# Optimization experiments

Hardware: AMD Instinct MI355X
Metric: run time of the kernel (lower is better)

The kernel has to match this reference:

```python
import math
import jax, jax.numpy as jnp
import numpy as np

B, S, H, E, F = 4, 2048, 1024, 8, 2048
CAPACITY_FACTOR = 1.25


def setup_inputs() -> dict:
    key = jax.random.key(0)
    ks = jax.random.split(key, 5)
    x = jax.random.normal(ks[0], (B, S, H), dtype=jnp.float32)
    gate_w = jax.random.normal(ks[1], (H, E), dtype=jnp.float32) * 0.02
    w1 = jax.random.normal(ks[2], (E, H, F), dtype=jnp.float32) * 0.02
    w2 = jax.random.normal(ks[3], (E, F, H), dtype=jnp.float32) * 0.02
    w3 = jax.random.normal(ks[4], (E, H, F), dtype=jnp.float32) * 0.02
    return {"x": x, "gate_w": gate_w, "w1": w1, "w2": w2, "w3": w3}


def reference(x, gate_w, w1, w2, w3):
    b, s, h = x.shape
    T = b * s
    e = gate_w.shape[1]
    xf = x.reshape(T, h)                           # [T, H]
    logits = xf @ gate_w                           # [T, E]
    capacity = min(math.ceil(T / e * CAPACITY_FACTOR), T)
    # Expert-choice: each expert picks its top-`capacity` tokens.
    scores, idx = jax.lax.top_k(logits.T, capacity)  # both [E, C]
    # Per-expert softmax over the selected tokens (dim=0 of the column vector in torch == capacity axis here).
    weights = jax.nn.softmax(scores, axis=1)       # [E, C]
    gathered = xf[idx]                             # [E, C, H]
    # Grouped SwiGLU FFN
    a = jnp.einsum('ech,ehf->ecf', gathered, w1)
    g = jnp.einsum('ech,ehf->ecf', gathered, w3)
    hidden = jax.nn.silu(a) * g                    # [E, C, F]
    out_e = jnp.einsum('ecf,efh->ech', hidden, w2) # [E, C, H]
    out_e = out_e * weights[..., None]
    # Weighted scatter-add combine
    yf = jnp.zeros((T, h), dtype=x.dtype).at[idx.reshape(-1)].add(
        out_e.reshape(-1, h))
    return yf.reshape(b, s, h), jnp.float32(0.0)
```

## Files before the change

### kernel.cpp

```cpp
#include <hip/hip_runtime.h>
#include <stdint.h>

typedef unsigned short ushort_t;
typedef __bf16 bf16x8 __attribute__((ext_vector_type(8)));
typedef float f32x4 __attribute__((ext_vector_type(4)));

#define T_TOK 8192
#define HDIM  1024
#define EXP   8
#define FDIM  2048
#define CAP   1280

__device__ __forceinline__ unsigned short f2b(float f) {
  unsigned u = __float_as_uint(f);
  u = (u + 0x7fffu + ((u >> 16) & 1u)) >> 16;
  return (unsigned short)u;
}
__device__ __forceinline__ unsigned pk2(unsigned short lo, unsigned short hi) {
  return (unsigned)lo | ((unsigned)hi << 16);
}
__device__ __forceinline__ unsigned map_u(float f) {
  unsigned u = __float_as_uint(f);
  return (u & 0x80000000u) ? ~u : (u | 0x80000000u);
}
__device__ __forceinline__ float unmap_f(unsigned m) {
  unsigned u = (m & 0x80000000u) ? (m ^ 0x80000000u) : ~m;
  return __uint_as_float(u);
}
__device__ __forceinline__ void gl_lds16(const void* g, void* l) {
  __builtin_amdgcn_global_load_lds((__attribute__((address_space(1))) void*)g,
                                   (__attribute__((address_space(3))) void*)l,
                                   16, 0, 0);
}

__global__ void __launch_bounds__(256) gate_cast_k(
    const float* __restrict__ x, const float* __restrict__ gw,
    float* __restrict__ logitsT, ushort_t* __restrict__ xb)
{
  int wave = threadIdx.x >> 6, lane = threadIdx.x & 63;
  int t = blockIdx.x * 4 + wave;
  const float* xr = x + (size_t)t * HDIM;
  ushort_t* xbr = xb + (size_t)t * HDIM;
  float acc[8];
#pragma unroll
  for (int i = 0; i < 8; ++i) acc[i] = 0.f;
#pragma unroll
  for (int i = 0; i < 16; ++i) {
    int h = i * 64 + lane;
    float xv = xr[h];
    xbr[h] = f2b(xv);
    const float4* g4 = (const float4*)(gw + (size_t)h * EXP);
    float4 lo = g4[0], hi = g4[1];
    acc[0] += xv * lo.x; acc[1] += xv * lo.y; acc[2] += xv * lo.z; acc[3] += xv * lo.w;
    acc[4] += xv * hi.x; acc[5] += xv * hi.y; acc[6] += xv * hi.z; acc[7] += xv * hi.w;
  }
#pragma unroll
  for (int off = 32; off > 0; off >>= 1) {
#pragma unroll
    for (int i = 0; i < 8; ++i) acc[i] += __shfl_xor(acc[i], off, 64);
  }
  if (lane == 0) {
#pragma unroll
    for (int i = 0; i < 8; ++i) logitsT[(size_t)i * T_TOK + t] = acc[i];
  }
}

__global__ void __launch_bounds__(256) select_k(
    const float* __restrict__ logitsT,
    unsigned* __restrict__ thr, int* __restrict__ needo, unsigned* __restrict__ umax)
{
  __shared__ int hist[256];
  __shared__ int ssum[256];
  __shared__ unsigned s_pref;
  __shared__ int s_rem;
  __shared__ unsigned smx[4];
  int e = blockIdx.x, tid = threadIdx.x;
  const float* base = logitsT + (size_t)e * T_TOK;

  unsigned m[32];
  unsigned mmax = 0;
#pragma unroll
  for (int i = 0; i < 32; ++i) {
    m[i] = map_u(base[tid + i * 256]);
    mmax = m[i] > mmax ? m[i] : mmax;
  }
#pragma unroll
  for (int off = 32; off > 0; off >>= 1) {
    unsigned o = __shfl_xor(mmax, off, 64);
    mmax = o > mmax ? o : mmax;
  }
  int lane = tid & 63, wv = tid >> 6;
  if (lane == 0) smx[wv] = mmax;
  if (tid == 0) { s_pref = 0; s_rem = CAP; }
  __syncthreads();
  if (tid == 0) {
    unsigned a = smx[0] > smx[1] ? smx[0] : smx[1];
    unsigned b = smx[2] > smx[3] ? smx[2] : smx[3];
    umax[e] = a > b ? a : b;
  }

  for (int r = 0; r < 4; ++r) {
    hist[tid] = 0;
    __syncthreads();
    unsigned pref = s_pref;
    int rem = s_rem;
    int shift = 24 - 8 * r;
#pragma unroll
    for (int i = 0; i < 32; ++i) {
      unsigned u = m[i];
      bool ok = (r == 0) || ((u >> (shift + 8)) == (pref >> (shift + 8)));
      if (ok) atomicAdd(&hist[(u >> shift) & 255], 1);
    }
    __syncthreads();
    ssum[tid] = hist[tid];
    __syncthreads();
    for (int st = 1; st < 256; st <<= 1) {
      int add = (tid + st < 256) ? ssum[tid + st] : 0;
      __syncthreads();
      ssum[tid] += add;
      __syncthreads();
    }
    int above = (tid < 255) ? ssum[tid + 1] : 0;
    if (ssum[tid] >= rem && above < rem) {
      s_pref = pref | ((unsigned)tid << shift);
      s_rem = rem - above;
    }
    __syncthreads();
  }
  if (tid == 0) { thr[e] = s_pref; needo[e] = s_rem; }
}

__global__ void __launch_bounds__(256) emit_k(
    const float* __restrict__ logitsT,
    const unsigned* __restrict__ thr, const int* __restrict__ needv,
    const unsigned* __restrict__ umaxv,
    int* __restrict__ idxo, float* __restrict__ exo,
    int* __restrict__ cnt, int* __restrict__ tie, float* __restrict__ expsum,
    int* __restrict__ tok_cnt, int* __restrict__ tok_ent)
{
  int t = blockIdx.x * 256 + threadIdx.x;
  int lane = threadIdx.x & 63;
  int lc = 0;
  int ents[8];
#pragma unroll
  for (int e = 0; e < EXP; ++e) {
    float f = logitsT[(size_t)e * T_TOK + t];
    unsigned u = map_u(f);
    unsigned te = thr[e];
    float fm = unmap_f(umaxv[e]);
    float v = __expf(f - fm);
    bool sel = u > te;
    unsigned long long mask = __ballot(sel);
    int nsel = __popcll(mask);
    int base = 0;
    if (lane == 0 && nsel) base = atomicAdd(&cnt[e], nsel);
    base = __shfl(base, 0, 64);
    int slot = -1;
    if (sel) slot = base + __popcll(mask & ((1ull << lane) - 1ull));
    if (u == te) {
      int k = atomicAdd(&tie[e], 1);
      if (k < needv[e]) {
        slot = atomicAdd(&cnt[e], 1);
        atomicAdd(&expsum[e], v);
      }
    }
    if (slot >= 0) {
      idxo[e * CAP + slot] = t;
      exo[e * CAP + slot] = v;
      ents[lc++] = (e << 16) | slot;
    }
    float vs = sel ? v : 0.f;
#pragma unroll
    for (int off = 32; off > 0; off >>= 1) vs += __shfl_xor(vs, off, 64);
    if (lane == 0 && vs != 0.f) atomicAdd(&expsum[e], vs);
  }
  tok_cnt[t] = lc;
  for (int i = 0; i < lc; ++i) tok_ent[t * 8 + i] = ents[i];
}

__global__ void __launch_bounds__(256) transpose3_k(
    const float* __restrict__ w1, const float* __restrict__ w3, const float* __restrict__ w2,
    ushort_t* __restrict__ w1t, ushort_t* __restrict__ w3t, ushort_t* __restrict__ w2t)
{
  __shared__ float tile[64][65];
  int b = blockIdx.x;
  const float* in; ushort_t* out; int R, Cc;
  if (b < 4096)      { in = w1; out = w1t; R = HDIM; Cc = FDIM; }
  else if (b < 8192) { in = w3; out = w3t; R = HDIM; Cc = FDIM; b -= 4096; }
  else               { in = w2; out = w2t; R = FDIM; Cc = HDIM; b -= 8192; }
  int tilesC = Cc >> 6;
  int tilesPer = (R >> 6) * tilesC;
  int e = b / tilesPer;
  int tb = b - e * tilesPer;
  int rt = tb / tilesC, ct = tb - rt * tilesC;
  const float* src = in + (size_t)e * R * Cc;
  ushort_t* dst = out + (size_t)e * R * Cc;
  int tr = threadIdx.x >> 4, tc = threadIdx.x & 15;
#pragma unroll
  for (int it = 0; it < 4; ++it) {
    int r = (rt << 6) + (it << 4) + tr;
    int c = (ct << 6) + (tc << 2);
    float4 v = *(const float4*)(src + (size_t)r * Cc + c);
    tile[(it << 4) + tr][(tc << 2) + 0] = v.x;
    tile[(it << 4) + tr][(tc << 2) + 1] = v.y;
    tile[(it << 4) + tr][(tc << 2) + 2] = v.z;
    tile[(it << 4) + tr][(tc << 2) + 3] = v.w;
  }
  __syncthreads();
#pragma unroll
  for (int it = 0; it < 4; ++it) {
    int cl = (it << 4) + tr;
    int rl = tc << 2;
    unsigned lo = pk2(f2b(tile[rl + 0][cl]), f2b(tile[rl + 1][cl]));
    unsigned hi = pk2(f2b(tile[rl + 2][cl]), f2b(tile[rl + 3][cl]));
    unsigned long long v = (unsigned long long)lo | ((unsigned long long)hi << 32);
    *(unsigned long long*)(dst + (size_t)((ct << 6) + cl) * R + (rt << 6) + rl) = v;
  }
}

__global__ void __launch_bounds__(256) gemm1_swiglu_k(
    const ushort_t* __restrict__ xb,
    const ushort_t* __restrict__ w1t,
    const ushort_t* __restrict__ w3t,
    const int* __restrict__ idx,
    ushort_t* __restrict__ hidden)
{
  int b = blockIdx.x;
  int ni_ = b & 7; int t1 = b >> 3; int mt = t1 % 10; int t2 = t1 / 10;
  int ng = t2 & 3; int e = t2 >> 2;
  int nt = ng * 8 + ni_;

  __shared__ __bf16 Alds[128 * 64];
  __shared__ __bf16 B1lds[64 * 64];
  __shared__ __bf16 B3lds[64 * 64];

  int tid = threadIdx.x;
  int lane = tid & 63, wave = tid >> 6;
  int wm = wave & 1, wn = wave >> 1;
  int l15 = lane & 15, quad = lane >> 4;

  int kc = tid & 7;
  int r0 = tid >> 3;
  const int* idxe = idx + e * CAP + mt * 128;
  const ushort_t* a_ptr[4];
#pragma unroll
  for (int j = 0; j < 4; ++j) {
    int row = r0 + j * 32;
    a_ptr[j] = xb + (size_t)idxe[row] * HDIM + ((kc ^ (row & 7)) * 8);
  }
  const ushort_t* wb1 = w1t + ((size_t)e * FDIM + nt * 64) * HDIM;
  const ushort_t* wb3 = w3t + ((size_t)e * FDIM + nt * 64) * HDIM;
  const ushort_t* b1_ptr[2];
  const ushort_t* b3_ptr[2];
#pragma unroll
  for (int j = 0; j < 2; ++j) {
    int row = r0 + j * 32;
    size_t off = (size_t)row * HDIM + ((kc ^ (row & 7)) * 8);
    b1_ptr[j] = wb1 + off;
    b3_ptr[j] = wb3 + off;
  }

  f32x4 acc1[4][2], acc3[4][2];
#pragma unroll
  for (int i = 0; i < 4; ++i)
#pragma unroll
    for (int j = 0; j < 2; ++j) {
      acc1[i][j] = (f32x4){0.f, 0.f, 0.f, 0.f};
      acc3[i][j] = (f32x4){0.f, 0.f, 0.f, 0.f};
    }

  for (int kt = 0; kt < HDIM / 64; ++kt) {
#pragma unroll
    for (int j = 0; j < 4; ++j) gl_lds16(a_ptr[j], Alds + ((size_t)tid + j * 256) * 8);
#pragma unroll
    for (int j = 0; j < 2; ++j) {
      gl_lds16(b1_ptr[j], B1lds + ((size_t)tid + j * 256) * 8);
      gl_lds16(b3_ptr[j], B3lds + ((size_t)tid + j * 256) * 8);
    }
    __syncthreads();
#pragma unroll
    for (int kh = 0; kh < 2; ++kh) {
      bf16x8 af[4], bf1[2], bf3[2];
#pragma unroll
      for (int i = 0; i < 4; ++i) {
        int row = wm * 64 + i * 16 + l15;
        af[i] = *(const bf16x8*)(Alds + row * 64 + (((kh * 4 + quad) ^ (row & 7)) * 8));
      }
#pragma unroll
      for (int j = 0; j < 2; ++j) {
        int row = wn * 32 + j * 16 + l15;
        int o = row * 64 + (((kh * 4 + quad) ^ (row & 7)) * 8);
        bf1[j] = *(const bf16x8*)(B1lds + o);
        bf3[j] = *(const bf16x8*)(B3lds + o);
      }
#pragma unroll
      for (int mi = 0; mi < 4; ++mi)
#pragma unroll
        for (int nj = 0; nj < 2; ++nj) {
          acc1[mi][nj] = __builtin_amdgcn_mfma_f32_16x16x32_bf16(af[mi], bf1[nj], acc1[mi][nj], 0, 0, 0);
          acc3[mi][nj] = __builtin_amdgcn_mfma_f32_16x16x32_bf16(af[mi], bf3[nj], acc3[mi][nj], 0, 0, 0);
        }
    }
    __syncthreads();
#pragma unroll
    for (int j = 0; j < 4; ++j) a_ptr[j] += 64;
#pragma unroll
    for (int j = 0; j < 2; ++j) { b1_ptr[j] += 64; b3_ptr[j] += 64; }
  }

  ushort_t* hb = hidden + ((size_t)e * CAP + mt * 128) * FDIM + nt * 64;
#pragma unroll
  for (int mi = 0; mi < 4; ++mi)
#pragma unroll
    for (int nj = 0; nj < 2; ++nj)
#pragma unroll
      for (int r = 0; r < 4; ++r) {
        int row = wm * 64 + mi * 16 + quad * 4 + r;
        int col = wn * 32 + nj * 16 + l15;
        float v1 = acc1[mi][nj][r];
        float v3 = acc3[mi][nj][r];
        float s = (v1 / (1.f + __expf(-v1))) * v3;
        hb[(size_t)row * FDIM + col] = f2b(s);
      }
}

__global__ void __launch_bounds__(256) gemm2_k(
    const ushort_t* __restrict__ hidden,
    const ushort_t* __restrict__ w2t,
    const float* __restrict__ ex, const float* __restrict__ expsum,
    float* __restrict__ oute)
{
  int b = blockIdx.x;
  int nt = b & 7; int t1 = b >> 3; int mt = t1 % 10; int e = t1 / 10;

  __shared__ __bf16 Alds[128 * 64];
  __shared__ __bf16 Blds[128 * 64];
  __shared__ float wgts[128];

  int tid = threadIdx.x;
  int lane = tid & 63, wave = tid >> 6;
  int wm = wave & 1, wn = wave >> 1;
  int l15 = lane & 15, quad = lane >> 4;

  if (tid < 128) wgts[tid] = ex[e * CAP + mt * 128 + tid] / expsum[e];

  int kc = tid & 7;
  int r0 = tid >> 3;
  const ushort_t* a_ptr[4];
  const ushort_t* b_ptr[4];
#pragma unroll
  for (int j = 0; j < 4; ++j) {
    int row = r0 + j * 32;
    a_ptr[j] = hidden + ((size_t)e * CAP + mt * 128 + row) * FDIM + ((kc ^ (row & 7)) * 8);
    b_ptr[j] = w2t + ((size_t)e * HDIM + nt * 128 + row) * FDIM + ((kc ^ (row & 7)) * 8);
  }

  f32x4 acc[4][4];
#pragma unroll
  for (int i = 0; i < 4; ++i)
#pragma unroll
    for (int j = 0; j < 4; ++j) acc[i][j] = (f32x4){0.f, 0.f, 0.f, 0.f};

  for (int kt = 0; kt < FDIM / 64; ++kt) {
#pragma unroll
    for (int j = 0; j < 4; ++j) {
      gl_lds16(a_ptr[j], Alds + ((size_t)tid + j * 256) * 8);
      gl_lds16(b_ptr[j], Blds + ((size_t)tid + j * 256) * 8);
    }
    __syncthreads();
#pragma unroll
    for (int kh = 0; kh < 2; ++kh) {
      bf16x8 af[4], bf[4];
#pragma unroll
      for (int i = 0; i < 4; ++i) {
        int rowa = wm * 64 + i * 16 + l15;
        af[i] = *(const bf16x8*)(Alds + rowa * 64 + (((kh * 4 + quad) ^ (rowa & 7)) * 8));
        int rowb = wn * 64 + i * 16 + l15;
        bf[i] = *(const bf16x8*)(Blds + rowb * 64 + (((kh * 4 + quad) ^ (rowb & 7)) * 8));
      }
#pragma unroll
      for (int mi = 0; mi < 4; ++mi)
#pragma unroll
        for (int nj = 0; nj < 4; ++nj)
          acc[mi][nj] = __builtin_amdgcn_mfma_f32_16x16x32_bf16(af[mi], bf[nj], acc[mi][nj], 0, 0, 0);
    }
    __syncthreads();
#pragma unroll
    for (int j = 0; j < 4; ++j) { a_ptr[j] += 64; b_ptr[j] += 64; }
  }

  float* ob = oute + ((size_t)e * CAP + mt * 128) * HDIM + nt * 128;
#pragma unroll
  for (int mi = 0; mi < 4; ++mi)
#pragma unroll
    for (int nj = 0; nj < 4; ++nj)
#pragma unroll
      for (int r = 0; r < 4; ++r) {
        int row = wm * 64 + mi * 16 + quad * 4 + r;
        int col = wn * 64 + nj * 16 + l15;
        ob[(size_t)row * HDIM + col] = acc[mi][nj][r] * wgts[row];
      }
}

__global__ void __launch_bounds__(256) combine_k(
    const float* __restrict__ oute,
    const int* __restrict__ tok_cnt, const int* __restrict__ tok_ent,
    float* __restrict__ y)
{
  int t = blockIdx.x;
  int c = threadIdx.x * 4;
  int n = tok_cnt[t];
  float4 acc = {0.f, 0.f, 0.f, 0.f};
  for (int i = 0; i < n; ++i) {
    int ent = tok_ent[t * 8 + i];
    int e = ent >> 16, slot = ent & 0xffff;
    float4 v = *(const float4*)(oute + (((size_t)e * CAP + slot) << 10) + c);
    acc.x += v.x; acc.y += v.y; acc.z += v.z; acc.w += v.w;
  }
  *(float4*)(y + ((size_t)t << 10) + c) = acc;
}

extern "C" void kernel_launch(void* const* d_in, const int* in_sizes, int n_in,
                              void* d_out, int out_size, void* d_ws, size_t ws_size,
                              hipStream_t stream)
{
  const float* x  = (const float*)d_in[0];
  const float* gw = (const float*)d_in[1];
  const float* w1 = (const float*)d_in[2];
  const float* w2 = (const float*)d_in[3];
  const float* w3 = (const float*)d_in[4];
  float* y = (float*)d_out;

  char* ws = (char*)d_ws;
  float*    logitsT = (float*)(ws + 0x0);
  int*      idx     = (int*)(ws + 0x40000);
  float*    exo     = (float*)(ws + 0x4A000);
  unsigned* thr    = (unsigned*)(ws + 0x54000);
  int*      need   = (int*)(ws + 0x54020);
  unsigned* umax   = (unsigned*)(ws + 0x54040);
  int*      cnt    = (int*)(ws + 0x54060);
  int*      tie    = (int*)(ws + 0x54080);
  float*    expsum = (float*)(ws + 0x540A0);
  int*      tok_cnt = (int*)(ws + 0x55000);
  int*      tok_ent = (int*)(ws + 0x5D000);
  ushort_t* xb     = (ushort_t*)(ws + 0xA0000);
  ushort_t* w1t    = (ushort_t*)(ws + 0x10A0000);
  ushort_t* w3t    = (ushort_t*)(ws + 0x30A0000);
  ushort_t* w2t    = (ushort_t*)(ws + 0x50A0000);
  ushort_t* hid    = (ushort_t*)(ws + 0x70A0000);
  float*    oute   = (float*)(ws + 0x10A0000);

  size_t yelems = (size_t)T_TOK * HDIM;
  if ((size_t)out_size > yelems)
    hipMemsetAsync((char*)d_out + yelems * 4, 0, ((size_t)out_size - yelems) * 4, stream);
  hipMemsetAsync(ws + 0x54000, 0, 256, stream);

  transpose3_k<<<3 * 4096, 256, 0, stream>>>(w1, w3, w2, w1t, w3t, w2t);
  gate_cast_k<<<T_TOK / 4, 256, 0, stream>>>(x, gw, logitsT, xb);
  select_k<<<EXP, 256, 0, stream>>>(logitsT, thr, need, umax);
  emit_k<<<T_TOK / 256, 256, 0, stream>>>(logitsT, thr, need, umax, idx, exo, cnt, tie, expsum, tok_cnt, tok_ent);
  gemm1_swiglu_k<<<EXP * 4 * 10 * 8, 256, 0, stream>>>(xb, w1t, w3t, idx, hid);
  gemm2_k<<<EXP * 10 * 8, 256, 0, stream>>>(hid, w2t, exo, expsum, oute);
  combine_k<<<T_TOK, 256, 0, stream>>>(oute, tok_cnt, tok_ent, y);
}
```

Measured before the change: 485.1 us.

## Double-buffer LDS tiles in both expert GEMM kernels to overlap loads with MFMA

Both the gate/up SwiGLU GEMM and the down-projection GEMM now keep two LDS buffers per operand. Each K-step issues the async global-to-LDS copies for the next tile before running the MFMAs on the current tile. This removes one barrier per iteration and hides global load latency behind compute. In exchange, LDS use per block doubles, which can lower the number of resident blocks per CU.

```diff
diff --git a/kernel.cpp b/kernel.cpp
--- a/kernel.cpp
+++ b/kernel.cpp
@@ -230,9 +230,9 @@
   int ng = t2 & 3; int e = t2 >> 2;
   int nt = ng * 8 + ni_;
 
-  __shared__ __bf16 Alds[128 * 64];
-  __shared__ __bf16 B1lds[64 * 64];
-  __shared__ __bf16 B3lds[64 * 64];
+  __shared__ __bf16 Alds[2][128 * 64];
+  __shared__ __bf16 B1lds[2][64 * 64];
+  __shared__ __bf16 B3lds[2][64 * 64];
 
   int tid = threadIdx.x;
   int lane = tid & 63, wave = tid >> 6;
@@ -269,29 +269,59 @@
       acc3[i][j] = (f32x4){0.f, 0.f, 0.f, 0.f};
     }
 
-  for (int kt = 0; kt < HDIM / 64; ++kt) {
-#pragma unroll
-    for (int j = 0; j < 4; ++j) gl_lds16(a_ptr[j], Alds + ((size_t)tid + j * 256) * 8);
-#pragma unroll
-    for (int j = 0; j < 2; ++j) {
-      gl_lds16(b1_ptr[j], B1lds + ((size_t)tid + j * 256) * 8);
-      gl_lds16(b3_ptr[j], B3lds + ((size_t)tid + j * 256) * 8);
-    }
-    __syncthreads();
+#pragma unroll
+  for (int j = 0; j < 4; ++j) gl_lds16(a_ptr[j], Alds[0] + ((size_t)tid + j * 256) * 8);
+#pragma unroll
+  for (int j = 0; j < 2; ++j) {
+    gl_lds16(b1_ptr[j], B1lds[0] + ((size_t)tid + j * 256) * 8);
+    gl_lds16(b3_ptr[j], B3lds[0] + ((size_t)tid + j * 256) * 8);
+  }
+#pragma unroll
+  for (int j = 0; j < 4; ++j) a_ptr[j] += 64;
+#pragma unroll
+  for (int j = 0; j < 2; ++j) { b1_ptr[j] += 64; b3_ptr[j] += 64; }
+  __syncthreads();
+
+  const int NT = HDIM / 64;
+  int cur = 0;
+  for (int kt = 0; kt < NT; ++kt) {
+    const __bf16* Ac  = Alds[cur];
+    const __bf16* B1c = B1lds[cur];
+    const __bf16* B3c = B3lds[cur];
+    __bf16* An  = Alds[cur ^ 1];
+    __bf16* B1n = B1lds[cur ^ 1];
+    __bf16* B3n = B3lds[cur ^ 1];
+
+    if (kt + 1 < NT) {
+#pragma unroll
+      for (int j = 0; j < 4; ++j) gl_lds16(a_ptr[j], An + ((size_t)tid + j * 256) * 8);
+#pragma unroll
+      for (int j = 0; j < 2; ++j) {
+        gl_lds16(b1_ptr[j], B1n + ((size_t)tid + j * 256) * 8);
+        gl_lds16(b3_ptr[j], B3n + ((size_t)tid + j * 256) * 8);
+      }
+      if (kt + 2 < NT) {
+#pragma unroll
+        for (int j = 0; j < 4; ++j) a_ptr[j] += 64;
+#pragma unroll
+        for (int j = 0; j < 2; ++j) { b1_ptr[j] += 64; b3_ptr[j] += 64; }
+      }
+    }
+
 #pragma unroll
     for (int kh = 0; kh < 2; ++kh) {
       bf16x8 af[4], bf1[2], bf3[2];
 #pragma unroll
       for (int i = 0; i < 4; ++i) {
         int row = wm * 64 + i * 16 + l15;
-        af[i] = *(const bf16x8*)(Alds + row * 64 + (((kh * 4 + quad) ^ (row & 7)) * 8));
+        af[i] = *(const bf16x8*)(Ac + row * 64 + (((kh * 4 + quad) ^ (row & 7)) * 8));
       }
 #pragma unroll
       for (int j = 0; j < 2; ++j) {
         int row = wn * 32 + j * 16 + l15;
         int o = row * 64 + (((kh * 4 + quad) ^ (row & 7)) * 8);
-        bf1[j] = *(const bf16x8*)(B1lds + o);
-        bf3[j] = *(const bf16x8*)(B3lds + o);
+        bf1[j] = *(const bf16x8*)(B1c + o);
+        bf3[j] = *(const bf16x8*)(B3c + o);
       }
 #pragma unroll
       for (int mi = 0; mi < 4; ++mi)
@@ -302,10 +332,7 @@
         }
     }
     __syncthreads();
-#pragma unroll
-    for (int j = 0; j < 4; ++j) a_ptr[j] += 64;
-#pragma unroll
-    for (int j = 0; j < 2; ++j) { b1_ptr[j] += 64; b3_ptr[j] += 64; }
+    cur ^= 1;
   }
 
   ushort_t* hb = hidden + ((size_t)e * CAP + mt * 128) * FDIM + nt * 64;
@@ -333,8 +360,8 @@
   int b = blockIdx.x;
   int nt = b & 7; int t1 = b >> 3; int mt = t1 % 10; int e = t1 / 10;
 
-  __shared__ __bf16 Alds[128 * 64];
-  __shared__ __bf16 Blds[128 * 64];
+  __shared__ __bf16 Alds[2][128 * 64];
+  __shared__ __bf16 Blds[2][128 * 64];
   __shared__ float wgts[128];
 
   int tid = threadIdx.x;
@@ -361,22 +388,44 @@
 #pragma unroll
     for (int j = 0; j < 4; ++j) acc[i][j] = (f32x4){0.f, 0.f, 0.f, 0.f};
 
-  for (int kt = 0; kt < FDIM / 64; ++kt) {
-#pragma unroll
-    for (int j = 0; j < 4; ++j) {
-      gl_lds16(a_ptr[j], Alds + ((size_t)tid + j * 256) * 8);
-      gl_lds16(b_ptr[j], Blds + ((size_t)tid + j * 256) * 8);
-    }
-    __syncthreads();
+#pragma unroll
+  for (int j = 0; j < 4; ++j) {
+    gl_lds16(a_ptr[j], Alds[0] + ((size_t)tid + j * 256) * 8);
+    gl_lds16(b_ptr[j], Blds[0] + ((size_t)tid + j * 256) * 8);
+  }
+#pragma unroll
+  for (int j = 0; j < 4; ++j) { a_ptr[j] += 64; b_ptr[j] += 64; }
+  __syncthreads();
+
+  const int NT = FDIM / 64;
+  int cur = 0;
+  for (int kt = 0; kt < NT; ++kt) {
+    const __bf16* Ac = Alds[cur];
+    const __bf16* Bc = Blds[cur];
+    __bf16* An = Alds[cur ^ 1];
+    __bf16* Bn = Blds[cur ^ 1];
+
+    if (kt + 1 < NT) {
+#pragma unroll
+      for (int j = 0; j < 4; ++j) {
+        gl_lds16(a_ptr[j], An + ((size_t)tid + j * 256) * 8);
+        gl_lds16(b_ptr[j], Bn + ((size_t)tid + j * 256) * 8);
+      }
+      if (kt + 2 < NT) {
+#pragma unroll
+        for (int j = 0; j < 4; ++j) { a_ptr[j] += 64; b_ptr[j] += 64; }
+      }
+    }
+
 #pragma unroll
     for (int kh = 0; kh < 2; ++kh) {
       bf16x8 af[4], bf[4];
 #pragma unroll
       for (int i = 0; i < 4; ++i) {
         int rowa = wm * 64 + i * 16 + l15;
-        af[i] = *(const bf16x8*)(Alds + rowa * 64 + (((kh * 4 + quad) ^ (rowa & 7)) * 8));
+        af[i] = *(const bf16x8*)(Ac + rowa * 64 + (((kh * 4 + quad) ^ (rowa & 7)) * 8));
         int rowb = wn * 64 + i * 16 + l15;
-        bf[i] = *(const bf16x8*)(Blds + rowb * 64 + (((kh * 4 + quad) ^ (rowb & 7)) * 8));
+        bf[i] = *(const bf16x8*)(Bc + rowb * 64 + (((kh * 4 + quad) ^ (rowb & 7)) * 8));
       }
 #pragma unroll
       for (int mi = 0; mi < 4; ++mi)
@@ -385,8 +434,7 @@
           acc[mi][nj] = __builtin_amdgcn_mfma_f32_16x16x32_bf16(af[mi], bf[nj], acc[mi][nj], 0, 0, 0);
     }
     __syncthreads();
-#pragma unroll
-    for (int j = 0; j < 4; ++j) { a_ptr[j] += 64; b_ptr[j] += 64; }
+    cur ^= 1;
   }
 
   float* ob = oute + ((size_t)e * CAP + mt * 128) * HDIM + nt * 128;
```

Measured after the change: 504.1 us. 3.9% more time.

## Pipeline gemm1 with triple-buffered LDS and double-buffer gemm2 loads

Applied to the files above, without the earlier changes.

gemm1 is restructured to use 512-thread blocks covering 256 tokens by 64 F columns. It streams K in 32-wide slices through a three-stage LDS ring, synchronised with explicit vmcnt waits and barriers, and raises wave priority around the MFMA bursts. gemm2 gains a second LDS buffer so the next K tile is loaded while the current one is computed, which removes one barrier per iteration. The intent is to hide global-load latency behind MFMA work, at the cost of more LDS per block and therefore possibly lower occupancy.

```diff
diff --git a/kernel.cpp b/kernel.cpp
--- a/kernel.cpp
+++ b/kernel.cpp
@@ -218,7 +218,33 @@
   }
 }
 
-__global__ void __launch_bounds__(256) gemm1_swiglu_k(
+#define G1_STAGE(BB) \
+  gl_lds16(pA0, lds + (BB)*12288 + (size_t)tid*8); \
+  gl_lds16(pA1, lds + (BB)*12288 + 4096 + (size_t)tid*8); \
+  gl_lds16(pB , lds + (BB)*12288 + 8192 + (size_t)tid*8);
+
+#define G1_ITER(CB, PB, VM, PREF) { \
+  asm volatile("s_waitcnt vmcnt(" VM ")" ::: "memory"); \
+  __builtin_amdgcn_s_barrier(); \
+  if (PREF) { G1_STAGE(PB); pA0 += 32; pA1 += 32; pB += 32; } \
+  bf16x8 af[4], b1v[2], b3v[2]; \
+  _Pragma("unroll") \
+  for (int mi = 0; mi < 4; ++mi) af[mi] = *(const bf16x8*)(lds + (CB)*12288 + aoff[mi]); \
+  _Pragma("unroll") \
+  for (int nj = 0; nj < 2; ++nj) { \
+    b1v[nj] = *(const bf16x8*)(lds + (CB)*12288 + b1off[nj]); \
+    b3v[nj] = *(const bf16x8*)(lds + (CB)*12288 + b1off[nj] + 2048); } \
+  __builtin_amdgcn_s_setprio(1); \
+  _Pragma("unroll") \
+  for (int mi = 0; mi < 4; ++mi) \
+    _Pragma("unroll") \
+    for (int nj = 0; nj < 2; ++nj) { \
+      acc1[mi][nj] = __builtin_amdgcn_mfma_f32_16x16x32_bf16(af[mi], b1v[nj], acc1[mi][nj], 0, 0, 0); \
+      acc3[mi][nj] = __builtin_amdgcn_mfma_f32_16x16x32_bf16(af[mi], b3v[nj], acc3[mi][nj], 0, 0, 0); } \
+  __builtin_amdgcn_s_setprio(0); \
+}
+
+__global__ void __launch_bounds__(512) gemm1_swiglu_k(
     const ushort_t* __restrict__ xb,
     const ushort_t* __restrict__ w1t,
     const ushort_t* __restrict__ w3t,
@@ -226,38 +252,43 @@
     ushort_t* __restrict__ hidden)
 {
   int b = blockIdx.x;
-  int ni_ = b & 7; int t1 = b >> 3; int mt = t1 % 10; int t2 = t1 / 10;
-  int ng = t2 & 3; int e = t2 >> 2;
-  int nt = ng * 8 + ni_;
-
-  __shared__ __bf16 Alds[128 * 64];
-  __shared__ __bf16 B1lds[64 * 64];
-  __shared__ __bf16 B3lds[64 * 64];
+  int ft = b & 31; int t1 = b >> 5; int mt = t1 % 5; int e = t1 / 5;
+  int f0 = ft * 64;
+
+  __shared__ __bf16 lds[3 * 12288];
 
   int tid = threadIdx.x;
   int lane = tid & 63, wave = tid >> 6;
-  int wm = wave & 1, wn = wave >> 1;
+  int wm = wave >> 1;
+  int wn = wave & 1;
   int l15 = lane & 15, quad = lane >> 4;
 
-  int kc = tid & 7;
-  int r0 = tid >> 3;
-  const int* idxe = idx + e * CAP + mt * 128;
-  const ushort_t* a_ptr[4];
-#pragma unroll
-  for (int j = 0; j < 4; ++j) {
-    int row = r0 + j * 32;
-    a_ptr[j] = xb + (size_t)idxe[row] * HDIM + ((kc ^ (row & 7)) * 8);
-  }
-  const ushort_t* wb1 = w1t + ((size_t)e * FDIM + nt * 64) * HDIM;
-  const ushort_t* wb3 = w3t + ((size_t)e * FDIM + nt * 64) * HDIM;
-  const ushort_t* b1_ptr[2];
-  const ushort_t* b3_ptr[2];
-#pragma unroll
-  for (int j = 0; j < 2; ++j) {
-    int row = r0 + j * 32;
-    size_t off = (size_t)row * HDIM + ((kc ^ (row & 7)) * 8);
-    b1_ptr[j] = wb1 + off;
-    b3_ptr[j] = wb3 + off;
+  int srow = tid >> 2;
+  int chunk = tid & 3;
+  int s_sw = (srow & 3) ^ ((srow >> 2) & 3);
+  int g_chunk = ((chunk ^ s_sw) * 8);
+
+  const int* idxe = idx + e * CAP + mt * 256;
+  int tok0 = idxe[srow];
+  int tok1 = idxe[srow + 128];
+  const ushort_t* pA0 = xb + (size_t)tok0 * HDIM + g_chunk;
+  const ushort_t* pA1 = xb + (size_t)tok1 * HDIM + g_chunk;
+  const ushort_t* pB = (srow < 64)
+      ? (w1t + ((size_t)e * FDIM + f0 + srow) * HDIM + g_chunk)
+      : (w3t + ((size_t)e * FDIM + f0 + (srow - 64)) * HDIM + g_chunk);
+
+  int aoff[4], b1off[2];
+#pragma unroll
+  for (int mi = 0; mi < 4; ++mi) {
+    int R = wm * 64 + mi * 16 + l15;
+    int sw = (R & 3) ^ ((R >> 2) & 3);
+    aoff[mi] = R * 32 + ((quad ^ sw) * 8);
+  }
+#pragma unroll
+  for (int nj = 0; nj < 2; ++nj) {
+    int r1 = wn * 32 + nj * 16 + l15;
+    int sw = (r1 & 3) ^ ((r1 >> 2) & 3);
+    b1off[nj] = 8192 + r1 * 32 + ((quad ^ sw) * 8);
   }
 
   f32x4 acc1[4][2], acc3[4][2];
@@ -269,46 +300,18 @@
       acc3[i][j] = (f32x4){0.f, 0.f, 0.f, 0.f};
     }
 
-  for (int kt = 0; kt < HDIM / 64; ++kt) {
-#pragma unroll
-    for (int j = 0; j < 4; ++j) gl_lds16(a_ptr[j], Alds + ((size_t)tid + j * 256) * 8);
-#pragma unroll
-    for (int j = 0; j < 2; ++j) {
-      gl_lds16(b1_ptr[j], B1lds + ((size_t)tid + j * 256) * 8);
-      gl_lds16(b3_ptr[j], B3lds + ((size_t)tid + j * 256) * 8);
-    }
-    __syncthreads();
-#pragma unroll
-    for (int kh = 0; kh < 2; ++kh) {
-      bf16x8 af[4], bf1[2], bf3[2];
-#pragma unroll
-      for (int i = 0; i < 4; ++i) {
-        int row = wm * 64 + i * 16 + l15;
-        af[i] = *(const bf16x8*)(Alds + row * 64 + (((kh * 4 + quad) ^ (row & 7)) * 8));
-      }
-#pragma unroll
-      for (int j = 0; j < 2; ++j) {
-        int row = wn * 32 + j * 16 + l15;
-        int o = row * 64 + (((kh * 4 + quad) ^ (row & 7)) * 8);
-        bf1[j] = *(const bf16x8*)(B1lds + o);
-        bf3[j] = *(const bf16x8*)(B3lds + o);
-      }
-#pragma unroll
-      for (int mi = 0; mi < 4; ++mi)
-#pragma unroll
-        for (int nj = 0; nj < 2; ++nj) {
-          acc1[mi][nj] = __builtin_amdgcn_mfma_f32_16x16x32_bf16(af[mi], bf1[nj], acc1[mi][nj], 0, 0, 0);
-          acc3[mi][nj] = __builtin_amdgcn_mfma_f32_16x16x32_bf16(af[mi], bf3[nj], acc3[mi][nj], 0, 0, 0);
-        }
-    }
-    __syncthreads();
-#pragma unroll
-    for (int j = 0; j < 4; ++j) a_ptr[j] += 64;
-#pragma unroll
-    for (int j = 0; j < 2; ++j) { b1_ptr[j] += 64; b3_ptr[j] += 64; }
-  }
-
-  ushort_t* hb = hidden + ((size_t)e * CAP + mt * 128) * FDIM + nt * 64;
+  G1_STAGE(0); pA0 += 32; pA1 += 32; pB += 32;
+  G1_STAGE(1); pA0 += 32; pA1 += 32; pB += 32;
+
+  for (int it = 0; it < 10; ++it) {
+    G1_ITER(0, 2, "3", 1)
+    G1_ITER(1, 0, "3", 1)
+    G1_ITER(2, 1, "3", 1)
+  }
+  G1_ITER(0, 0, "3", 0)
+  G1_ITER(1, 0, "0", 0)
+
+  ushort_t* hb = hidden + ((size_t)e * CAP + mt * 256) * FDIM + f0;
 #pragma unroll
   for (int mi = 0; mi < 4; ++mi)
 #pragma unroll
@@ -333,8 +336,8 @@
   int b = blockIdx.x;
   int nt = b & 7; int t1 = b >> 3; int mt = t1 % 10; int e = t1 / 10;
 
-  __shared__ __bf16 Alds[128 * 64];
-  __shared__ __bf16 Blds[128 * 64];
+  __shared__ __bf16 Alds[2][128 * 64];
+  __shared__ __bf16 Blds[2][128 * 64];
   __shared__ float wgts[128];
 
   int tid = threadIdx.x;
@@ -361,22 +364,44 @@
 #pragma unroll
     for (int j = 0; j < 4; ++j) acc[i][j] = (f32x4){0.f, 0.f, 0.f, 0.f};
 
-  for (int kt = 0; kt < FDIM / 64; ++kt) {
-#pragma unroll
-    for (int j = 0; j < 4; ++j) {
-      gl_lds16(a_ptr[j], Alds + ((size_t)tid + j * 256) * 8);
-      gl_lds16(b_ptr[j], Blds + ((size_t)tid + j * 256) * 8);
-    }
-    __syncthreads();
+#pragma unroll
+  for (int j = 0; j < 4; ++j) {
+    gl_lds16(a_ptr[j], Alds[0] + ((size_t)tid + j * 256) * 8);
+    gl_lds16(b_ptr[j], Blds[0] + ((size_t)tid + j * 256) * 8);
+  }
+#pragma unroll
+  for (int j = 0; j < 4; ++j) { a_ptr[j] += 64; b_ptr[j] += 64; }
+  __syncthreads();
+
+  const int NT = FDIM / 64;
+  int cur = 0;
+  for (int kt = 0; kt < NT; ++kt) {
+    const __bf16* Ac = Alds[cur];
+    const __bf16* Bc = Blds[cur];
+    __bf16* An = Alds[cur ^ 1];
+    __bf16* Bn = Blds[cur ^ 1];
+
+    if (kt + 1 < NT) {
+#pragma unroll
+      for (int j = 0; j < 4; ++j) {
+        gl_lds16(a_ptr[j], An + ((size_t)tid + j * 256) * 8);
+        gl_lds16(b_ptr[j], Bn + ((size_t)tid + j * 256) * 8);
+      }
+      if (kt + 2 < NT) {
+#pragma unroll
+        for (int j = 0; j < 4; ++j) { a_ptr[j] += 64; b_ptr[j] += 64; }
+      }
+    }
+
 #pragma unroll
     for (int kh = 0; kh < 2; ++kh) {
       bf16x8 af[4], bf[4];
 #pragma unroll
       for (int i = 0; i < 4; ++i) {
         int rowa = wm * 64 + i * 16 + l15;
-        af[i] = *(const bf16x8*)(Alds + rowa * 64 + (((kh * 4 + quad) ^ (rowa & 7)) * 8));
+        af[i] = *(const bf16x8*)(Ac + rowa * 64 + (((kh * 4 + quad) ^ (rowa & 7)) * 8));
         int rowb = wn * 64 + i * 16 + l15;
-        bf[i] = *(const bf16x8*)(Blds + rowb * 64 + (((kh * 4 + quad) ^ (rowb & 7)) * 8));
+        bf[i] = *(const bf16x8*)(Bc + rowb * 64 + (((kh * 4 + quad) ^ (rowb & 7)) * 8));
       }
 #pragma unroll
       for (int mi = 0; mi < 4; ++mi)
@@ -385,8 +410,7 @@
           acc[mi][nj] = __builtin_amdgcn_mfma_f32_16x16x32_bf16(af[mi], bf[nj], acc[mi][nj], 0, 0, 0);
     }
     __syncthreads();
-#pragma unroll
-    for (int j = 0; j < 4; ++j) { a_ptr[j] += 64; b_ptr[j] += 64; }
+    cur ^= 1;
   }
 
   float* ob = oute + ((size_t)e * CAP + mt * 128) * HDIM + nt * 128;
@@ -459,7 +483,7 @@
   gate_cast_k<<<T_TOK / 4, 256, 0, stream>>>(x, gw, logitsT, xb);
   select_k<<<EXP, 256, 0, stream>>>(logitsT, thr, need, umax);
   emit_k<<<T_TOK / 256, 256, 0, stream>>>(logitsT, thr, need, umax, idx, exo, cnt, tie, expsum, tok_cnt, tok_ent);
-  gemm1_swiglu_k<<<EXP * 4 * 10 * 8, 256, 0, stream>>>(xb, w1t, w3t, idx, hid);
+  gemm1_swiglu_k<<<EXP * 5 * 32, 512, 0, stream>>>(xb, w1t, w3t, idx, hid);
   gemm2_k<<<EXP * 10 * 8, 256, 0, stream>>>(hid, w2t, exo, expsum, oute);
   combine_k<<<T_TOK, 256, 0, stream>>>(oute, tok_cnt, tok_ent, y);
 }
```

Result: faster. 471.9 us (-2.7%).
